# Kernel tuning notes

Measured on AMD Instinct MI355X. Metric: run time of the kernel, lower is better.

## Reference

```python
import jax, jax.numpy as jnp
import numpy as np

NPOINT, RADIUS, NSAMPLE = 1024, 0.2, 32
EPS = 1e-5


def _fps(xyz, npoint):
    # Iterative farthest point sampling (deterministic start at index 0).
    B, N, _ = xyz.shape
    def step(carry, _):
        distance, farthest = carry
        centroid = jnp.take_along_axis(xyz, farthest[:, None, None], axis=1)  # (B,1,3)
        d = jnp.sum((xyz - centroid) ** 2, -1)                                # (B,N)
        distance = jnp.minimum(distance, d)
        return (distance, jnp.argmax(distance, -1)), farthest
    init = (jnp.full((B, N), 1e10, xyz.dtype), jnp.zeros((B,), jnp.int32))
    _, idx = jax.lax.scan(step, init, None, length=npoint)
    return idx.T  # (B, npoint)


def _gather(points, idx):
    # points (B,N,C), idx (B,S,K) -> (B,S,K,C)
    B, S, K = idx.shape
    flat = jnp.take_along_axis(points, idx.reshape(B, S * K)[:, :, None], axis=1)
    return flat.reshape(B, S, K, points.shape[-1])


def _query_ball(xyz, new_xyz):
    # For each centroid, first NSAMPLE point indices within RADIUS (pad with first hit).
    B, N, _ = xyz.shape
    sqr = jnp.sum((new_xyz[:, :, None, :] - xyz[:, None, :, :]) ** 2, -1)  # (B,S,N)
    gi = jnp.where(sqr > RADIUS ** 2, N, jnp.arange(N, dtype=jnp.int32)[None, None, :])
    gi = jnp.sort(gi, axis=-1)[:, :, :NSAMPLE]
    return jnp.where(gi == N, gi[:, :, :1], gi)  # (B,S,K)


def _cond_layer(x, t_embed, wt, bt, wc, bc, g, b):
    # ConditionalConv1d: x += time_mlp(gelu(t)); 1x1 conv; BatchNorm (batch stats); GELU.
    tp = jax.nn.gelu(t_embed, approximate=False) @ wt.T + bt      # (B,Cin)
    x = x + tp[:, None, None, :]
    y = jnp.einsum('bskc,oc->bsko', x, wc) + bc                   # (B,S,K,Cout)
    mu = jnp.mean(y, axis=(0, 1, 2))
    var = jnp.var(y, axis=(0, 1, 2))
    y = (y - mu) * jax.lax.rsqrt(var + EPS) * g + b
    return jax.nn.gelu(y, approximate=False)


def _forward(xyz, points, t_embed, params):
    fps_idx = _fps(xyz, NPOINT)                                        # (B,S)
    new_xyz = jnp.take_along_axis(xyz, fps_idx[:, :, None], axis=1)    # (B,S,3)
    idx = _query_ball(xyz, new_xyz)                                    # (B,S,K)
    grouped_xyz = _gather(xyz, idx) - new_xyz[:, :, None, :]           # (B,S,K,3)
    grouped_pts = _gather(jnp.swapaxes(points, 1, 2), idx)             # (B,S,K,C)
    x = jnp.concatenate([grouped_xyz, grouped_pts], -1)                # (B,S,K,C+3)
    for p in params:
        x = _cond_layer(x, t_embed, *p)
    new_points = jnp.swapaxes(jnp.max(x, axis=2), 1, 2)                # (B,Cout,S)
    return new_xyz, new_points


def setup_inputs() -> dict:
    key = jax.random.key(0)
    ks = iter(jax.random.split(key, 32))
    B, N, CIN, T = 8, 4096, 64, 128
    chans = [(CIN + 3, 64), (64, 64), (64, 128)]
    inp = {
        "xyz": jax.random.normal(next(ks), (B, N, 3), jnp.float32),
        "points": jax.random.normal(next(ks), (B, CIN, N), jnp.float32),
        "t_embed": jax.random.normal(next(ks), (B, T), jnp.float32),
    }
    for i, (ci, co) in enumerate(chans):
        inp[f"wt{i}"] = jax.random.normal(next(ks), (ci, T), jnp.float32) * 0.05
        inp[f"bt{i}"] = jnp.zeros((ci,), jnp.float32)
        inp[f"wc{i}"] = jax.random.normal(next(ks), (co, ci), jnp.float32) * 0.1
        inp[f"bc{i}"] = jnp.zeros((co,), jnp.float32)
        inp[f"g{i}"] = jnp.ones((co,), jnp.float32)
        inp[f"be{i}"] = jnp.zeros((co,), jnp.float32)
    return inp


def reference(xyz, points, t_embed,
              wt0, bt0, wc0, bc0, g0, be0,
              wt1, bt1, wc1, bc1, g1, be1,
              wt2, bt2, wc2, bc2, g2, be2):
    params = [(wt0, bt0, wc0, bc0, g0, be0),
              (wt1, bt1, wc1, bc1, g1, be1),
              (wt2, bt2, wc2, bc2, g2, be2)]
    return _forward(xyz, points, t_embed, params)
```

## Files before the change

### kernel.cpp

```cpp
#include <hip/hip_runtime.h>
#include <cmath>

#define Bc 8
#define Nc 4096
#define Sc 1024
#define Kc 32
#define Mc (Bc*Sc*Kc)

typedef float v2f __attribute__((ext_vector_type(2)));

__device__ __forceinline__ float gelu_f(float x){
  return 0.5f*x*(1.0f + erff(x*0.70710678f));
}

__device__ __forceinline__ v2f pk_add(v2f a, v2f b){
  v2f d; asm("v_pk_add_f32 %0, %1, %2" : "=v"(d) : "v"(a), "v"(b)); return d;
}
__device__ __forceinline__ v2f pk_mul(v2f a, v2f b){
  v2f d; asm("v_pk_mul_f32 %0, %1, %2" : "=v"(d) : "v"(a), "v"(b)); return d;
}

#define ROR_MAXF(v, n) { int _t = __builtin_amdgcn_update_dpp(__float_as_int(v), __float_as_int(v), 0x120|(n), 0xF, 0xF, false); \
                         v = fmaxf(v, __int_as_float(_t)); }
#define BC15_MAXF(v)   { int _t = __builtin_amdgcn_update_dpp(__float_as_int(v), __float_as_int(v), 0x142, 0xA, 0xF, false); \
                         v = fmaxf(v, __int_as_float(_t)); }
#define BC31_MAXF(v)   { int _t = __builtin_amdgcn_update_dpp(__float_as_int(v), __float_as_int(v), 0x143, 0xC, 0xF, false); \
                         v = fmaxf(v, __int_as_float(_t)); }

#define TK(v_, i_) { const bool _t = ((v_) > Bv) || (((v_) == Bv) && ((i_) < Bi)); \
  Bv = _t ? (v_) : Bv; Bi = _t ? (i_) : Bi; }

__global__ __launch_bounds__(256) void fused_front_kernel(
    const float* __restrict__ xyz, float* __restrict__ new_xyz,
    const float* __restrict__ points, float* __restrict__ pointsT,
    const float* __restrict__ t_embed,
    const float* __restrict__ wt0, const float* __restrict__ bt0,
    const float* __restrict__ wt1, const float* __restrict__ bt1,
    const float* __restrict__ wt2, const float* __restrict__ bt2,
    float* __restrict__ tp)
{
  __shared__ __align__(16) float smem[17424];
  const int bid = blockIdx.x;
  const int tid = threadIdx.x;

  if (bid < 8){
    const int b = bid;
    const int lane = tid & 63;
    const int wv = tid >> 6;
    const float* xb = xyz + b*Nc*3;
    float*    skv   = smem;
    unsigned* ski   = (unsigned*)(smem + 8);
    int*      shist = (int*)(smem + 16);
    float4*   c4    = (float4*)(smem + 1040);

    const int base = tid << 4;
    float4 f[12];
    const float4* src = (const float4*)(xb + base*3);
#pragma unroll
    for (int q=0;q<12;++q) f[q] = src[q];
#define AR(i) ((i)%4==0 ? f[(i)/4].x : (i)%4==1 ? f[(i)/4].y : (i)%4==2 ? f[(i)/4].z : f[(i)/4].w)
    v2f px2[8], py2[8], pz2[8], d2[8];
#pragma unroll
    for (int k=0;k<8;++k){
      px2[k].x = AR(6*k+0); py2[k].x = AR(6*k+1); pz2[k].x = AR(6*k+2);
      px2[k].y = AR(6*k+3); py2[k].y = AR(6*k+4); pz2[k].y = AR(6*k+5);
      c4[base+2*k  ] = make_float4(px2[k].x, py2[k].x, pz2[k].x, 0.f);
      c4[base+2*k+1] = make_float4(px2[k].y, py2[k].y, pz2[k].y, 0.f);
      d2[k].x = 1e10f; d2[k].y = 1e10f;
    }
#undef AR
    __syncthreads();
    int widx = 0;
    for (int it=0; it<Sc; ++it){
      const float4 cc = c4[widx];
      if (tid==0) shist[it] = widx;
      v2f ncx, ncy, ncz;
      ncx.x=-cc.x; ncx.y=-cc.x; ncy.x=-cc.y; ncy.y=-cc.y; ncz.x=-cc.z; ncz.y=-cc.z;
      float bvx=-1.0f, bvy=-1.0f;
#pragma unroll
      for (int k=0;k<8;++k){
        const v2f dx = pk_add(px2[k], ncx);
        const v2f dy = pk_add(py2[k], ncy);
        const v2f dz = pk_add(pz2[k], ncz);
        const v2f dd = pk_add(pk_add(pk_mul(dx,dx), pk_mul(dy,dy)), pk_mul(dz,dz));
        v2f dn;
        dn.x = fminf(d2[k].x, dd.x);
        dn.y = fminf(d2[k].y, dd.y);
        d2[k] = dn;
        bvx = fmaxf(bvx, dn.x);
        bvy = fmaxf(bvy, dn.y);
      }
      const float bv = fmaxf(bvx, bvy);
      unsigned bi_local = 0xFFFFFFFFu;
#pragma unroll
      for (int k=0;k<8;++k){
        const unsigned c0 = (d2[k].x == bv) ? (unsigned)(base + 2*k    ) : 0xFFFFFFFFu;
        const unsigned c1 = (d2[k].y == bv) ? (unsigned)(base + 2*k + 1) : 0xFFFFFFFFu;
        const unsigned cm = (c0 < c1) ? c0 : c1;
        bi_local = (cm < bi_local) ? cm : bi_local;
      }
      float mv = bv;
      ROR_MAXF(mv,1); ROR_MAXF(mv,2); ROR_MAXF(mv,4); ROR_MAXF(mv,8);
      BC15_MAXF(mv); BC31_MAXF(mv);
      mv = __int_as_float(__builtin_amdgcn_readlane(__float_as_int(mv), 63));
      const unsigned long long mk = __ballot(bv == mv);
      const int src_lane = __ffsll(mk) - 1;
      const unsigned bi = (unsigned)__builtin_amdgcn_readlane((int)bi_local, src_lane);
      const int p4 = (it & 1) << 2;
      if (lane==0){ skv[p4+wv] = mv; ski[p4+wv] = bi; }
      __syncthreads();
      const float4 m4 = *reinterpret_cast<const float4*>(&skv[p4]);
      const uint4  i4 = *reinterpret_cast<const uint4*>(&ski[p4]);
      float Bv = m4.x; unsigned Bi = i4.x;
      TK(m4.y, i4.y) TK(m4.z, i4.z) TK(m4.w, i4.w)
      widx = (int)Bi;
    }
    __syncthreads();
    for (int i = tid; i < Sc; i += 256){
      const float4 cc = c4[shist[i]];
      float* o = new_xyz + ((size_t)b*Sc + i)*3;
      o[0]=cc.x; o[1]=cc.y; o[2]=cc.z;
    }
  } else if (bid < 520){
    const int t  = bid - 8;
    const int tb = t >> 6;
    const int n0 = (t & 63) << 6;
    float (*tile)[65] = (float(*)[65])smem;
    const int sub = tid >> 6;
    const int ln  = tid & 63;
#pragma unroll 4
    for (int cp=0; cp<16; ++cp){
      const int c = (cp<<2) + sub;
      tile[c][ln] = points[((size_t)(tb*64+c))*Nc + n0 + ln];
    }
    __syncthreads();
#pragma unroll 4
    for (int np=0; np<16; ++np){
      const int nl = (np<<2) + sub;
      pointsT[((size_t)(tb*Nc + n0 + nl))*64 + ln] = tile[ln][nl];
    }
  } else {
    float* ge = smem;
    for (int i = tid; i < Bc*128; i += 256) ge[i] = gelu_f(t_embed[i]);
    __syncthreads();
    for (int i = tid; i < 3*Bc*68; i += 256){
      const int l = i / (Bc*68);
      const int r = i - l*(Bc*68);
      const int b = r / 68;
      const int c = r - b*68;
      const int ci = (l==0) ? 67 : 64;
      float v = 0.0f;
      if (c < ci){
        const float* wt = (l==0)?wt0:((l==1)?wt1:wt2);
        const float* bt = (l==0)?bt0:((l==1)?bt1:bt2);
        const float* w = wt + c*128;
        const float* g = ge + b*128;
        float acc = 0.0f;
        for (int t2=0;t2<128;++t2) acc = fmaf(g[t2], w[t2], acc);
        v = acc + bt[c];
      }
      tp[i] = v;
    }
  }
}

__global__ __launch_bounds__(256) void ballgather_kernel(const float* __restrict__ xyz,
    const float* __restrict__ new_xyz, const float* __restrict__ pointsT,
    float* __restrict__ X){
  const int g = (blockIdx.x<<2) + (threadIdx.x>>6);
  const int lane = threadIdx.x & 63;
  const int w = threadIdx.x >> 6;
  const int b = g >> 10;
  const float* xb = xyz + b*Nc*3;
  const float cx = new_xyz[g*3+0];
  const float cy = new_xyz[g*3+1];
  const float cz = new_xyz[g*3+2];
  __shared__ int sidx[4][32];
  int total = 0;
  for (int base=0; base<Nc; base+=64){
    const int i = base + lane;
    float dx=__fsub_rn(cx, xb[i*3+0]);
    float dy=__fsub_rn(cy, xb[i*3+1]);
    float dz=__fsub_rn(cz, xb[i*3+2]);
    float sq=__fadd_rn(__fadd_rn(__fmul_rn(dx,dx),__fmul_rn(dy,dy)),__fmul_rn(dz,dz));
    bool hit = !(sq > 0.04f);
    unsigned long long m = __ballot(hit);
    if (hit){
      int pos = total + (int)__popcll(m & ((1ull<<lane)-1ull));
      if (pos < 32) sidx[w][pos] = i;
    }
    total += (int)__popcll(m);
    if (total >= 32) break;
  }
  const int fill = (total < 32) ? total : 32;
  const int first = sidx[w][0];
  if (lane >= fill && lane < 32) sidx[w][lane] = first;
  for (int k=0; k<32; ++k){
    const int pidx = sidx[w][k];
    const float* pt = pointsT + ((size_t)((b<<12)+pidx))*64;
    float* xr = X + (size_t)((g<<5)+k)*68;
    float v;
    if      (lane==0) v = __fsub_rn(xb[pidx*3+0], cx);
    else if (lane==1) v = __fsub_rn(xb[pidx*3+1], cy);
    else if (lane==2) v = __fsub_rn(xb[pidx*3+2], cz);
    else              v = pt[lane-3];
    xr[lane] = v;
    if (lane < 4){
      const int c = 64 + lane;
      xr[c] = (c<67) ? pt[c-3] : 0.0f;
    }
  }
}

template<int NORMIN, int CI_REAL, int CI_PAD, int LDX>
__global__ __launch_bounds__(256) void mm_kernel(const float* X,
    const float* __restrict__ wc, const float* __restrict__ tp,
    const float* __restrict__ sc_in, const float* __restrict__ sh_in,
    float* Y, float* __restrict__ pS, float* __restrict__ pQ, int o_base)
{
  __shared__ __align__(16) float wT[CI_PAD][64];
  __shared__ __align__(16) float tpr[CI_PAD];
  __shared__ __align__(16) float scN[64], shN[64];
  __shared__ float redS[4][64];
  __shared__ float redQ[4][64];
  const int tid = threadIdx.x;
  const int m0 = blockIdx.x << 8;
  const int b  = blockIdx.x >> 7;
  for (int idx = tid; idx < CI_PAD*64; idx += 256){
    int c = idx >> 6, o = idx & 63;
    wT[c][o] = (c < CI_REAL) ? wc[(o_base + o)*CI_REAL + c] : 0.0f;
  }
  if (tid < CI_PAD) tpr[tid] = tp[b*68 + tid];
  if (NORMIN && tid < 64){ scN[tid] = sc_in[tid]; shN[tid] = sh_in[tid]; }
  __syncthreads();
  const int rg = tid >> 2, cg = tid & 3;
  const float* x0 = X + (size_t)(m0 + (rg<<2)) * LDX;
  float4 acc[4][4];
#pragma unroll
  for (int r=0;r<4;++r)
#pragma unroll
    for (int q=0;q<4;++q) acc[r][q] = make_float4(0.f,0.f,0.f,0.f);

  float4 xpf[4];
#pragma unroll
  for (int r=0;r<4;++r) xpf[r] = *reinterpret_cast<const float4*>(x0 + r*LDX);

#pragma unroll 1
  for (int c = 0; c < CI_PAD; c += 4){
    float4 xc[4];
#pragma unroll
    for (int r=0;r<4;++r) xc[r] = xpf[r];
    if (c + 4 < CI_PAD){
#pragma unroll
      for (int r=0;r<4;++r) xpf[r] = *reinterpret_cast<const float4*>(x0 + r*LDX + (c+4));
    }
    const float4 tpv = *reinterpret_cast<const float4*>(&tpr[c]);
    if (NORMIN){
      const float4 sci = *reinterpret_cast<const float4*>(&scN[c]);
      const float4 shi = *reinterpret_cast<const float4*>(&shN[c]);
#pragma unroll
      for (int r=0;r<4;++r){
        xc[r].x = gelu_f(fmaf(xc[r].x, sci.x, shi.x));
        xc[r].y = gelu_f(fmaf(xc[r].y, sci.y, shi.y));
        xc[r].z = gelu_f(fmaf(xc[r].z, sci.z, shi.z));
        xc[r].w = gelu_f(fmaf(xc[r].w, sci.w, shi.w));
      }
    }
    float4 xr[4];
#pragma unroll
    for (int r=0;r<4;++r)
      xr[r] = make_float4(xc[r].x+tpv.x, xc[r].y+tpv.y, xc[r].z+tpv.z, xc[r].w+tpv.w);
#pragma unroll
    for (int cc=0; cc<4; ++cc){
      const float* wrow = &wT[c+cc][cg<<4];
      const float4 w0 = *reinterpret_cast<const float4*>(wrow);
      const float4 w1 = *reinterpret_cast<const float4*>(wrow+4);
      const float4 w2 = *reinterpret_cast<const float4*>(wrow+8);
      const float4 w3 = *reinterpret_cast<const float4*>(wrow+12);
#pragma unroll
      for (int r=0;r<4;++r){
        const float xs = (cc==0)?xr[r].x:((cc==1)?xr[r].y:((cc==2)?xr[r].z:xr[r].w));
        acc[r][0].x = fmaf(xs, w0.x, acc[r][0].x);
        acc[r][0].y = fmaf(xs, w0.y, acc[r][0].y);
        acc[r][0].z = fmaf(xs, w0.z, acc[r][0].z);
        acc[r][0].w = fmaf(xs, w0.w, acc[r][0].w);
        acc[r][1].x = fmaf(xs, w1.x, acc[r][1].x);
        acc[r][1].y = fmaf(xs, w1.y, acc[r][1].y);
        acc[r][1].z = fmaf(xs, w1.z, acc[r][1].z);
        acc[r][1].w = fmaf(xs, w1.w, acc[r][1].w);
        acc[r][2].x = fmaf(xs, w2.x, acc[r][2].x);
        acc[r][2].y = fmaf(xs, w2.y, acc[r][2].y);
        acc[r][2].z = fmaf(xs, w2.z, acc[r][2].z);
        acc[r][2].w = fmaf(xs, w2.w, acc[r][2].w);
        acc[r][3].x = fmaf(xs, w3.x, acc[r][3].x);
        acc[r][3].y = fmaf(xs, w3.y, acc[r][3].y);
        acc[r][3].z = fmaf(xs, w3.z, acc[r][3].z);
        acc[r][3].w = fmaf(xs, w3.w, acc[r][3].w);
      }
    }
  }
#pragma unroll
  for (int r=0;r<4;++r){
    float4* yp = reinterpret_cast<float4*>(Y + (size_t)(m0 + (rg<<2) + r)*64 + (cg<<4));
#pragma unroll
    for (int q=0;q<4;++q) yp[q] = acc[r][q];
  }
  float4 s[4], q2[4];
#pragma unroll
  for (int q=0;q<4;++q){
    float sx=0,sy=0,sz=0,sw=0, qx=0,qy=0,qz=0,qw=0;
#pragma unroll
    for (int r=0;r<4;++r){
      sx+=acc[r][q].x; qx+=acc[r][q].x*acc[r][q].x;
      sy+=acc[r][q].y; qy+=acc[r][q].y*acc[r][q].y;
      sz+=acc[r][q].z; qz+=acc[r][q].z*acc[r][q].z;
      sw+=acc[r][q].w; qw+=acc[r][q].w*acc[r][q].w;
    }
    s[q]=make_float4(sx,sy,sz,sw); q2[q]=make_float4(qx,qy,qz,qw);
  }
  const int lane = tid & 63, wvv = tid >> 6;
#pragma unroll
  for (int off=32; off>=4; off>>=1){
#pragma unroll
    for (int q=0;q<4;++q){
      s[q].x  += __shfl_down(s[q].x,  off);
      s[q].y  += __shfl_down(s[q].y,  off);
      s[q].z  += __shfl_down(s[q].z,  off);
      s[q].w  += __shfl_down(s[q].w,  off);
      q2[q].x += __shfl_down(q2[q].x, off);
      q2[q].y += __shfl_down(q2[q].y, off);
      q2[q].z += __shfl_down(q2[q].z, off);
      q2[q].w += __shfl_down(q2[q].w, off);
    }
  }
  if (lane < 4){
#pragma unroll
    for (int q=0;q<4;++q){
      redS[wvv][lane*16 + q*4 + 0] = s[q].x;
      redS[wvv][lane*16 + q*4 + 1] = s[q].y;
      redS[wvv][lane*16 + q*4 + 2] = s[q].z;
      redS[wvv][lane*16 + q*4 + 3] = s[q].w;
      redQ[wvv][lane*16 + q*4 + 0] = q2[q].x;
      redQ[wvv][lane*16 + q*4 + 1] = q2[q].y;
      redQ[wvv][lane*16 + q*4 + 2] = q2[q].z;
      redQ[wvv][lane*16 + q*4 + 3] = q2[q].w;
    }
  }
  __syncthreads();
  if (tid < 64){
    float a=0.f, bb=0.f;
#pragma unroll
    for (int w2=0; w2<4; ++w2){ a += redS[w2][tid]; bb += redQ[w2][tid]; }
    pS[(blockIdx.x<<6) + tid] = a;
    pQ[(blockIdx.x<<6) + tid] = bb;
  }
}

__global__ __launch_bounds__(256) void mm2_kernel(const float* X,
    const float* __restrict__ wc, const float* __restrict__ tp,
    const float* __restrict__ sc_in, const float* __restrict__ sh_in,
    float* Y0, float* Y1, float* __restrict__ pS, float* __restrict__ pQ)
{
  __shared__ __align__(16) float wT[64][128];
  __shared__ __align__(16) float tpr[64];
  __shared__ __align__(16) float scN[64], shN[64];
  __shared__ float redS[4][128];
  __shared__ float redQ[4][128];
  const int tid = threadIdx.x;
  const int m0 = blockIdx.x << 7;
  const int b  = blockIdx.x >> 8;
  for (int idx = tid; idx < 64*128; idx += 256){
    const int c = idx >> 7, o = idx & 127;
    wT[c][o] = wc[o*64 + c];
  }
  if (tid < 64) tpr[tid] = tp[b*68 + tid];
  else if (tid < 128) scN[tid-64] = sc_in[tid-64];
  else if (tid < 192) shN[tid-128] = sh_in[tid-128];
  __syncthreads();
  const int rg = tid >> 2, cg = tid & 3;
  const int cb = cg << 2;
  const float* x0 = X + (size_t)(m0 + (rg<<1)) * 64;
  float4 acc[2][8];
#pragma unroll
  for (int r=0;r<2;++r)
#pragma unroll
    for (int q=0;q<8;++q) acc[r][q] = make_float4(0.f,0.f,0.f,0.f);

  float4 xpf[2];
  xpf[0] = *reinterpret_cast<const float4*>(x0);
  xpf[1] = *reinterpret_cast<const float4*>(x0 + 64);

#pragma unroll 1
  for (int c = 0; c < 64; c += 4){
    float4 xc[2]; xc[0]=xpf[0]; xc[1]=xpf[1];
    if (c + 4 < 64){
      xpf[0] = *reinterpret_cast<const float4*>(x0 + (c+4));
      xpf[1] = *reinterpret_cast<const float4*>(x0 + 64 + (c+4));
    }
    const float4 tpv = *reinterpret_cast<const float4*>(&tpr[c]);
    const float4 sci = *reinterpret_cast<const float4*>(&scN[c]);
    const float4 shi = *reinterpret_cast<const float4*>(&shN[c]);
#pragma unroll
    for (int r=0;r<2;++r){
      xc[r].x = gelu_f(fmaf(xc[r].x, sci.x, shi.x)) + tpv.x;
      xc[r].y = gelu_f(fmaf(xc[r].y, sci.y, shi.y)) + tpv.y;
      xc[r].z = gelu_f(fmaf(xc[r].z, sci.z, shi.z)) + tpv.z;
      xc[r].w = gelu_f(fmaf(xc[r].w, sci.w, shi.w)) + tpv.w;
    }
#pragma unroll
    for (int cc=0; cc<4; ++cc){
      const float xs0 = (cc==0)?xc[0].x:((cc==1)?xc[0].y:((cc==2)?xc[0].z:xc[0].w));
      const float xs1 = (cc==0)?xc[1].x:((cc==1)?xc[1].y:((cc==2)?xc[1].z:xc[1].w));
      const float* wrow = &wT[c+cc][cb];
#pragma unroll
      for (int j=0;j<8;++j){
        const float4 wv = *reinterpret_cast<const float4*>(wrow + (j<<4));
        acc[0][j].x = fmaf(xs0, wv.x, acc[0][j].x);
        acc[0][j].y = fmaf(xs0, wv.y, acc[0][j].y);
        acc[0][j].z = fmaf(xs0, wv.z, acc[0][j].z);
        acc[0][j].w = fmaf(xs0, wv.w, acc[0][j].w);
        acc[1][j].x = fmaf(xs1, wv.x, acc[1][j].x);
        acc[1][j].y = fmaf(xs1, wv.y, acc[1][j].y);
        acc[1][j].z = fmaf(xs1, wv.z, acc[1][j].z);
        acc[1][j].w = fmaf(xs1, wv.w, acc[1][j].w);
      }
    }
  }
#pragma unroll
  for (int r=0;r<2;++r){
    const size_t row = (size_t)(m0 + (rg<<1) + r);
#pragma unroll
    for (int j=0;j<8;++j){
      float* yb = (j<4) ? Y0 : Y1;
      const int col = ((j<4) ? (j<<4) : ((j-4)<<4)) + cb;
      *reinterpret_cast<float4*>(yb + row*64 + col) = acc[r][j];
    }
  }
  const int lane = tid & 63, wvv = tid >> 6;
#pragma unroll
  for (int j=0;j<8;++j){
    float4 s = make_float4(acc[0][j].x+acc[1][j].x, acc[0][j].y+acc[1][j].y,
                           acc[0][j].z+acc[1][j].z, acc[0][j].w+acc[1][j].w);
    float4 q2 = make_float4(acc[0][j].x*acc[0][j].x + acc[1][j].x*acc[1][j].x,
                            acc[0][j].y*acc[0][j].y + acc[1][j].y*acc[1][j].y,
                            acc[0][j].z*acc[0][j].z + acc[1][j].z*acc[1][j].z,
                            acc[0][j].w*acc[0][j].w + acc[1][j].w*acc[1][j].w);
#pragma unroll
    for (int off=32; off>=4; off>>=1){
      s.x += __shfl_down(s.x, off);   s.y += __shfl_down(s.y, off);
      s.z += __shfl_down(s.z, off);   s.w += __shfl_down(s.w, off);
      q2.x += __shfl_down(q2.x, off); q2.y += __shfl_down(q2.y, off);
      q2.z += __shfl_down(q2.z, off); q2.w += __shfl_down(q2.w, off);
    }
    if (lane < 4){
      const int ch = (j<<4) + (lane<<2);
      redS[wvv][ch+0]=s.x;  redS[wvv][ch+1]=s.y;  redS[wvv][ch+2]=s.z;  redS[wvv][ch+3]=s.w;
      redQ[wvv][ch+0]=q2.x; redQ[wvv][ch+1]=q2.y; redQ[wvv][ch+2]=q2.z; redQ[wvv][ch+3]=q2.w;
    }
  }
  __syncthreads();
  if (tid < 128){
    float a=0.f, bb=0.f;
#pragma unroll
    for (int w2=0; w2<4; ++w2){ a += redS[w2][tid]; bb += redQ[w2][tid]; }
    pS[(size_t)blockIdx.x*128 + tid] = a;
    pQ[(size_t)blockIdx.x*128 + tid] = bb;
  }
}

template<int CO>
__global__ __launch_bounds__(1024) void finalize_kernel(const float* __restrict__ pS,
    const float* __restrict__ pQ, const float* __restrict__ g, const float* __restrict__ be,
    float* __restrict__ scale, float* __restrict__ shift, int nblk){
  __shared__ float rS[1024], rQ[1024];
  constexpr int NCH = 1024 / CO;
  const int o  = threadIdx.x & (CO-1);
  const int ch = threadIdx.x / CO;
  const int per = nblk / NCH;
  const int i0 = ch * per;
  float s=0.f, q=0.f;
#pragma unroll 4
  for (int i=0;i<per;++i){
    s += pS[(size_t)(i0+i)*CO + o];
    q += pQ[(size_t)(i0+i)*CO + o];
  }
  rS[threadIdx.x]=s; rQ[threadIdx.x]=q;
  __syncthreads();
  if (threadIdx.x < CO){
    float ss = 0.f, qq = 0.f;
#pragma unroll
    for (int c=0;c<NCH;++c){ ss += rS[c*CO+o]; qq += rQ[c*CO+o]; }
    const float inv_n = 1.0f/(float)Mc;
    const float mu = ss*inv_n;
    const float var = qq*inv_n - mu*mu;
    const float rs = 1.0f/sqrtf(var + 1e-5f);
    const float sc = rs*g[o];
    scale[o] = sc;
    shift[o] = fmaf(-mu, sc, be[o]);
  }
}

__global__ __launch_bounds__(256) void pool_kernel(const float* __restrict__ Y,
    const float* __restrict__ scale, const float* __restrict__ shift,
    float* __restrict__ out, int o_base){
  __shared__ float pool[32][65];
  const int tid = threadIdx.x;
  const int b  = blockIdx.x >> 5;
  const int s0 = (blockIdx.x & 31) << 5;
  const int c  = tid & 63;
  const int sl0 = tid >> 6;
  const float sc = scale[c], sh = shift[c];
  for (int sp=0; sp<8; ++sp){
    const int sl = (sp<<2) + sl0;
    const int s = s0 + sl;
    const float* yp = Y + ((size_t)((b<<10)+s)<<5)*64 + c;
    float mx = -1e30f;
#pragma unroll 4
    for (int k=0;k<32;++k){
      float v = yp[(size_t)(k<<6)];
      v = gelu_f(fmaf(v, sc, sh));
      mx = fmaxf(mx, v);
    }
    pool[sl][c] = mx;
  }
  __syncthreads();
  for (int p=0;p<8;++p){
    const int c2 = (p<<3) + (tid>>5);
    const int sl = tid & 31;
    out[((size_t)((b<<7) + o_base + c2)<<10) + s0 + sl] = pool[sl][c2];
  }
}

extern "C" void kernel_launch(void* const* d_in, const int* in_sizes, int n_in,
                              void* d_out, int out_size, void* d_ws, size_t ws_size,
                              hipStream_t stream){
  const float* xyz     = (const float*)d_in[0];
  const float* points  = (const float*)d_in[1];
  const float* t_embed = (const float*)d_in[2];
  const float* wt0=(const float*)d_in[3],  *bt0=(const float*)d_in[4],  *wc0=(const float*)d_in[5];
  const float* g0 =(const float*)d_in[7],  *be0=(const float*)d_in[8];
  const float* wt1=(const float*)d_in[9],  *bt1=(const float*)d_in[10], *wc1=(const float*)d_in[11];
  const float* g1 =(const float*)d_in[13], *be1=(const float*)d_in[14];
  const float* wt2=(const float*)d_in[15], *bt2=(const float*)d_in[16], *wc2=(const float*)d_in[17];
  const float* g2 =(const float*)d_in[19], *be2=(const float*)d_in[20];

  float* out_xyz = (float*)d_out;
  float* out_pts = (float*)d_out + Bc*Sc*3;

  float* ws       = (float*)d_ws;
  float* tp       = ws + 0;
  float* pointsT  = ws + 2048;
  float* pS       = ws + 2099200;
  float* X        = ws + 2361344;
  float* Ya       = ws + 20187136;
  float* pQ       = ws + 36964352;
  float* sc0      = ws + 37226496;
  float* sh0      = sc0 + 64;
  float* sc1      = sc0 + 128;
  float* sh1      = sc0 + 192;
  float* sc2      = sc0 + 256;
  float* sh2      = sc0 + 384;
  float* Yx       = X;

  const int NBLK = Mc/256;

  fused_front_kernel<<<521, 256, 0, stream>>>(xyz, out_xyz, points, pointsT,
      t_embed, wt0,bt0, wt1,bt1, wt2,bt2, tp);
  ballgather_kernel<<<(Bc*Sc)/4, 256, 0, stream>>>(xyz, out_xyz, pointsT, X);

  mm_kernel<0,67,68,68><<<NBLK, 256, 0, stream>>>(X, wc0, tp, nullptr, nullptr, Ya, pS, pQ, 0);
  finalize_kernel<64><<<1, 1024, 0, stream>>>(pS, pQ, g0, be0, sc0, sh0, NBLK);

  mm_kernel<1,64,64,64><<<NBLK, 256, 0, stream>>>(Ya, wc1, tp + 544, sc0, sh0, Ya, pS, pQ, 0);
  finalize_kernel<64><<<1, 1024, 0, stream>>>(pS, pQ, g1, be1, sc1, sh1, NBLK);

  mm2_kernel<<<Mc/128, 256, 0, stream>>>(Ya, wc2, tp + 1088, sc1, sh1, Yx, Ya, pS, pQ);
  finalize_kernel<128><<<1, 1024, 0, stream>>>(pS, pQ, g2, be2, sc2, sh2, Mc/128);

  pool_kernel<<<Bc*Sc/32, 256, 0, stream>>>(Yx, sc2,    sh2,    out_pts, 0);
  pool_kernel<<<Bc*Sc/32, 256, 0, stream>>>(Ya, sc2+64, sh2+64, out_pts, 64);
}
```

Baseline: 1.176 ms.

## Halve mm_kernel row tile, deepen X prefetch, merge pool launches

mm_kernel now has each block cover 128 rows, with 2 rows per thread instead of 4. That doubles the block count and cuts accumulator registers, aiming for more occupancy and better latency hiding. Both mm_kernel and mm2_kernel now prefetch two 4-channel chunks of X ahead instead of one, to overlap global loads with FMA work. The two pool_kernel launches become a single launch that picks its input half from the block index. In exchange, each weight value loaded from LDS now feeds fewer FMAs, and there are twice as many partial BN statistics for finalize to reduce.

```diff
diff --git a/kernel.cpp b/kernel.cpp
--- a/kernel.cpp
+++ b/kernel.cpp
@@ -212,6 +212,54 @@
   }
 }
 
+#define MM_CHUNK(CB, XV)                                                            \
+  {                                                                                 \
+    const float4 tpv = *reinterpret_cast<const float4*>(&tpr[CB]);                  \
+    if (NORMIN){                                                                    \
+      const float4 sci = *reinterpret_cast<const float4*>(&scN[CB]);                \
+      const float4 shi = *reinterpret_cast<const float4*>(&shN[CB]);                \
+      _Pragma("unroll")                                                             \
+      for (int r=0;r<2;++r){                                                        \
+        XV[r].x = gelu_f(fmaf(XV[r].x, sci.x, shi.x));                              \
+        XV[r].y = gelu_f(fmaf(XV[r].y, sci.y, shi.y));                              \
+        XV[r].z = gelu_f(fmaf(XV[r].z, sci.z, shi.z));                              \
+        XV[r].w = gelu_f(fmaf(XV[r].w, sci.w, shi.w));                              \
+      }                                                                             \
+    }                                                                               \
+    _Pragma("unroll")                                                               \
+    for (int r=0;r<2;++r){                                                          \
+      XV[r].x += tpv.x; XV[r].y += tpv.y; XV[r].z += tpv.z; XV[r].w += tpv.w;       \
+    }                                                                               \
+    _Pragma("unroll")                                                               \
+    for (int cc=0; cc<4; ++cc){                                                     \
+      const float* wrow = &wT[(CB)+cc][cg<<4];                                      \
+      const float4 w0 = *reinterpret_cast<const float4*>(wrow);                     \
+      const float4 w1 = *reinterpret_cast<const float4*>(wrow+4);                   \
+      const float4 w2 = *reinterpret_cast<const float4*>(wrow+8);                   \
+      const float4 w3 = *reinterpret_cast<const float4*>(wrow+12);                  \
+      _Pragma("unroll")                                                             \
+      for (int r=0;r<2;++r){                                                        \
+        const float xs = (cc==0)?XV[r].x:((cc==1)?XV[r].y:((cc==2)?XV[r].z:XV[r].w));\
+        acc[r][0].x = fmaf(xs, w0.x, acc[r][0].x);                                  \
+        acc[r][0].y = fmaf(xs, w0.y, acc[r][0].y);                                  \
+        acc[r][0].z = fmaf(xs, w0.z, acc[r][0].z);                                  \
+        acc[r][0].w = fmaf(xs, w0.w, acc[r][0].w);                                  \
+        acc[r][1].x = fmaf(xs, w1.x, acc[r][1].x);                                  \
+        acc[r][1].y = fmaf(xs, w1.y, acc[r][1].y);                                  \
+        acc[r][1].z = fmaf(xs, w1.z, acc[r][1].z);                                  \
+        acc[r][1].w = fmaf(xs, w1.w, acc[r][1].w);                                  \
+        acc[r][2].x = fmaf(xs, w2.x, acc[r][2].x);                                  \
+        acc[r][2].y = fmaf(xs, w2.y, acc[r][2].y);                                  \
+        acc[r][2].z = fmaf(xs, w2.z, acc[r][2].z);                                  \
+        acc[r][2].w = fmaf(xs, w2.w, acc[r][2].w);                                  \
+        acc[r][3].x = fmaf(xs, w3.x, acc[r][3].x);                                  \
+        acc[r][3].y = fmaf(xs, w3.y, acc[r][3].y);                                  \
+        acc[r][3].z = fmaf(xs, w3.z, acc[r][3].z);                                  \
+        acc[r][3].w = fmaf(xs, w3.w, acc[r][3].w);                                  \
+      }                                                                             \
+    }                                                                               \
+  }
+
 template<int NORMIN, int CI_REAL, int CI_PAD, int LDX>
 __global__ __launch_bounds__(256) void mm_kernel(const float* X,
     const float* __restrict__ wc, const float* __restrict__ tp,
@@ -224,8 +272,8 @@
   __shared__ float redS[4][64];
   __shared__ float redQ[4][64];
   const int tid = threadIdx.x;
-  const int m0 = blockIdx.x << 8;
-  const int b  = blockIdx.x >> 7;
+  const int m0 = blockIdx.x << 7;
+  const int b  = blockIdx.x >> 8;
   for (int idx = tid; idx < CI_PAD*64; idx += 256){
     int c = idx >> 6, o = idx & 63;
     wT[c][o] = (c < CI_REAL) ? wc[(o_base + o)*CI_REAL + c] : 0.0f;
@@ -234,89 +282,51 @@
   if (NORMIN && tid < 64){ scN[tid] = sc_in[tid]; shN[tid] = sh_in[tid]; }
   __syncthreads();
   const int rg = tid >> 2, cg = tid & 3;
-  const float* x0 = X + (size_t)(m0 + (rg<<2)) * LDX;
-  float4 acc[4][4];
-#pragma unroll
-  for (int r=0;r<4;++r)
+  const float* x0 = X + (size_t)(m0 + (rg<<1)) * LDX;
+  float4 acc[2][4];
+#pragma unroll
+  for (int r=0;r<2;++r)
 #pragma unroll
     for (int q=0;q<4;++q) acc[r][q] = make_float4(0.f,0.f,0.f,0.f);
 
-  float4 xpf[4];
-#pragma unroll
-  for (int r=0;r<4;++r) xpf[r] = *reinterpret_cast<const float4*>(x0 + r*LDX);
+  float4 pfA[2], pfB[2];
+  pfA[0] = *reinterpret_cast<const float4*>(x0);
+  pfA[1] = *reinterpret_cast<const float4*>(x0 + LDX);
+  pfB[0] = *reinterpret_cast<const float4*>(x0 + 4);
+  pfB[1] = *reinterpret_cast<const float4*>(x0 + LDX + 4);
 
 #pragma unroll 1
-  for (int c = 0; c < CI_PAD; c += 4){
-    float4 xc[4];
-#pragma unroll
-    for (int r=0;r<4;++r) xc[r] = xpf[r];
+  for (int c = 0; c < CI_PAD; c += 8){
+    float4 xa[2]; xa[0]=pfA[0]; xa[1]=pfA[1];
+    if (c + 8 < CI_PAD){
+      pfA[0] = *reinterpret_cast<const float4*>(x0 + (c+8));
+      pfA[1] = *reinterpret_cast<const float4*>(x0 + LDX + (c+8));
+    }
+    MM_CHUNK(c, xa)
     if (c + 4 < CI_PAD){
-#pragma unroll
-      for (int r=0;r<4;++r) xpf[r] = *reinterpret_cast<const float4*>(x0 + r*LDX + (c+4));
-    }
-    const float4 tpv = *reinterpret_cast<const float4*>(&tpr[c]);
-    if (NORMIN){
-      const float4 sci = *reinterpret_cast<const float4*>(&scN[c]);
-      const float4 shi = *reinterpret_cast<const float4*>(&shN[c]);
-#pragma unroll
-      for (int r=0;r<4;++r){
-        xc[r].x = gelu_f(fmaf(xc[r].x, sci.x, shi.x));
-        xc[r].y = gelu_f(fmaf(xc[r].y, sci.y, shi.y));
-        xc[r].z = gelu_f(fmaf(xc[r].z, sci.z, shi.z));
-        xc[r].w = gelu_f(fmaf(xc[r].w, sci.w, shi.w));
+      float4 xb2[2]; xb2[0]=pfB[0]; xb2[1]=pfB[1];
+      if (c + 12 < CI_PAD){
+        pfB[0] = *reinterpret_cast<const float4*>(x0 + (c+12));
+        pfB[1] = *reinterpret_cast<const float4*>(x0 + LDX + (c+12));
       }
-    }
-    float4 xr[4];
-#pragma unroll
-    for (int r=0;r<4;++r)
-      xr[r] = make_float4(xc[r].x+tpv.x, xc[r].y+tpv.y, xc[r].z+tpv.z, xc[r].w+tpv.w);
-#pragma unroll
-    for (int cc=0; cc<4; ++cc){
-      const float* wrow = &wT[c+cc][cg<<4];
-      const float4 w0 = *reinterpret_cast<const float4*>(wrow);
-      const float4 w1 = *reinterpret_cast<const float4*>(wrow+4);
-      const float4 w2 = *reinterpret_cast<const float4*>(wrow+8);
-      const float4 w3 = *reinterpret_cast<const float4*>(wrow+12);
-#pragma unroll
-      for (int r=0;r<4;++r){
-        const float xs = (cc==0)?xr[r].x:((cc==1)?xr[r].y:((cc==2)?xr[r].z:xr[r].w));
-        acc[r][0].x = fmaf(xs, w0.x, acc[r][0].x);
-        acc[r][0].y = fmaf(xs, w0.y, acc[r][0].y);
-        acc[r][0].z = fmaf(xs, w0.z, acc[r][0].z);
-        acc[r][0].w = fmaf(xs, w0.w, acc[r][0].w);
-        acc[r][1].x = fmaf(xs, w1.x, acc[r][1].x);
-        acc[r][1].y = fmaf(xs, w1.y, acc[r][1].y);
-        acc[r][1].z = fmaf(xs, w1.z, acc[r][1].z);
-        acc[r][1].w = fmaf(xs, w1.w, acc[r][1].w);
-        acc[r][2].x = fmaf(xs, w2.x, acc[r][2].x);
-        acc[r][2].y = fmaf(xs, w2.y, acc[r][2].y);
-        acc[r][2].z = fmaf(xs, w2.z, acc[r][2].z);
-        acc[r][2].w = fmaf(xs, w2.w, acc[r][2].w);
-        acc[r][3].x = fmaf(xs, w3.x, acc[r][3].x);
-        acc[r][3].y = fmaf(xs, w3.y, acc[r][3].y);
-        acc[r][3].z = fmaf(xs, w3.z, acc[r][3].z);
-        acc[r][3].w = fmaf(xs, w3.w, acc[r][3].w);
-      }
-    }
-  }
-#pragma unroll
-  for (int r=0;r<4;++r){
-    float4* yp = reinterpret_cast<float4*>(Y + (size_t)(m0 + (rg<<2) + r)*64 + (cg<<4));
+      MM_CHUNK(c+4, xb2)
+    }
+  }
+#pragma unroll
+  for (int r=0;r<2;++r){
+    float4* yp = reinterpret_cast<float4*>(Y + (size_t)(m0 + (rg<<1) + r)*64 + (cg<<4));
 #pragma unroll
     for (int q=0;q<4;++q) yp[q] = acc[r][q];
   }
   float4 s[4], q2[4];
 #pragma unroll
   for (int q=0;q<4;++q){
-    float sx=0,sy=0,sz=0,sw=0, qx=0,qy=0,qz=0,qw=0;
-#pragma unroll
-    for (int r=0;r<4;++r){
-      sx+=acc[r][q].x; qx+=acc[r][q].x*acc[r][q].x;
-      sy+=acc[r][q].y; qy+=acc[r][q].y*acc[r][q].y;
-      sz+=acc[r][q].z; qz+=acc[r][q].z*acc[r][q].z;
-      sw+=acc[r][q].w; qw+=acc[r][q].w*acc[r][q].w;
-    }
-    s[q]=make_float4(sx,sy,sz,sw); q2[q]=make_float4(qx,qy,qz,qw);
+    s[q]  = make_float4(acc[0][q].x+acc[1][q].x, acc[0][q].y+acc[1][q].y,
+                        acc[0][q].z+acc[1][q].z, acc[0][q].w+acc[1][q].w);
+    q2[q] = make_float4(acc[0][q].x*acc[0][q].x + acc[1][q].x*acc[1][q].x,
+                        acc[0][q].y*acc[0][q].y + acc[1][q].y*acc[1][q].y,
+                        acc[0][q].z*acc[0][q].z + acc[1][q].z*acc[1][q].z,
+                        acc[0][q].w*acc[0][q].w + acc[1][q].w*acc[1][q].w);
   }
   const int lane = tid & 63, wvv = tid >> 6;
 #pragma unroll
@@ -351,8 +361,8 @@
     float a=0.f, bb=0.f;
 #pragma unroll
     for (int w2=0; w2<4; ++w2){ a += redS[w2][tid]; bb += redQ[w2][tid]; }
-    pS[(blockIdx.x<<6) + tid] = a;
-    pQ[(blockIdx.x<<6) + tid] = bb;
+    pS[((size_t)blockIdx.x<<6) + tid] = a;
+    pQ[((size_t)blockIdx.x<<6) + tid] = bb;
   }
 }
 
@@ -386,45 +396,58 @@
 #pragma unroll
     for (int q=0;q<8;++q) acc[r][q] = make_float4(0.f,0.f,0.f,0.f);
 
-  float4 xpf[2];
-  xpf[0] = *reinterpret_cast<const float4*>(x0);
-  xpf[1] = *reinterpret_cast<const float4*>(x0 + 64);
+#define MM2_CHUNK(CB, XV)                                                          \
+  {                                                                                \
+    const float4 tpv = *reinterpret_cast<const float4*>(&tpr[CB]);                 \
+    const float4 sci = *reinterpret_cast<const float4*>(&scN[CB]);                 \
+    const float4 shi = *reinterpret_cast<const float4*>(&shN[CB]);                 \
+    _Pragma("unroll")                                                              \
+    for (int r=0;r<2;++r){                                                         \
+      XV[r].x = gelu_f(fmaf(XV[r].x, sci.x, shi.x)) + tpv.x;                       \
+      XV[r].y = gelu_f(fmaf(XV[r].y, sci.y, shi.y)) + tpv.y;                       \
+      XV[r].z = gelu_f(fmaf(XV[r].z, sci.z, shi.z)) + tpv.z;                       \
+      XV[r].w = gelu_f(fmaf(XV[r].w, sci.w, shi.w)) + tpv.w;                       \
+    }                                                                              \
+    _Pragma("unroll")                                                              \
+    for (int cc=0; cc<4; ++cc){                                                    \
+      const float xs0 = (cc==0)?XV[0].x:((cc==1)?XV[0].y:((cc==2)?XV[0].z:XV[0].w));\
+      const float xs1 = (cc==0)?XV[1].x:((cc==1)?XV[1].y:((cc==2)?XV[1].z:XV[1].w));\
+      const float* wrow = &wT[(CB)+cc][cb];                                        \
+      _Pragma("unroll")                                                            \
+      for (int j=0;j<8;++j){                                                       \
+        const float4 wv = *reinterpret_cast<const float4*>(wrow + (j<<4));         \
+        acc[0][j].x = fmaf(xs0, wv.x, acc[0][j].x);                                \
+        acc[0][j].y = fmaf(xs0, wv.y, acc[0][j].y);                                \
+        acc[0][j].z = fmaf(xs0, wv.z, acc[0][j].z);                                \
+        acc[0][j].w = fmaf(xs0, wv.w, acc[0][j].w);                                \
+        acc[1][j].x = fmaf(xs1, wv.x, acc[1][j].x);                                \
+        acc[1][j].y = fmaf(xs1, wv.y, acc[1][j].y);                                \
+        acc[1][j].z = fmaf(xs1, wv.z, acc[1][j].z);                                \
+        acc[1][j].w = fmaf(xs1, wv.w, acc[1][j].w);                                \
+      }                                                                            \
+    }                                                                              \
+  }
+
+  float4 pfA[2], pfB[2];
+  pfA[0] = *reinterpret_cast<const float4*>(x0);
+  pfA[1] = *reinterpret_cast<const float4*>(x0 + 64);
+  pfB[0] = *reinterpret_cast<const float4*>(x0 + 4);
+  pfB[1] = *reinterpret_cast<const float4*>(x0 + 64 + 4);
 
 #pragma unroll 1
-  for (int c = 0; c < 64; c += 4){
-    float4 xc[2]; xc[0]=xpf[0]; xc[1]=xpf[1];
-    if (c + 4 < 64){
-      xpf[0] = *reinterpret_cast<const float4*>(x0 + (c+4));
-      xpf[1] = *reinterpret_cast<const float4*>(x0 + 64 + (c+4));
-    }
-    const float4 tpv = *reinterpret_cast<const float4*>(&tpr[c]);
-    const float4 sci = *reinterpret_cast<const float4*>(&scN[c]);
-    const float4 shi = *reinterpret_cast<const float4*>(&shN[c]);
-#pragma unroll
-    for (int r=0;r<2;++r){
-      xc[r].x = gelu_f(fmaf(xc[r].x, sci.x, shi.x)) + tpv.x;
-      xc[r].y = gelu_f(fmaf(xc[r].y, sci.y, shi.y)) + tpv.y;
-      xc[r].z = gelu_f(fmaf(xc[r].z, sci.z, shi.z)) + tpv.z;
-      xc[r].w = gelu_f(fmaf(xc[r].w, sci.w, shi.w)) + tpv.w;
-    }
-#pragma unroll
-    for (int cc=0; cc<4; ++cc){
-      const float xs0 = (cc==0)?xc[0].x:((cc==1)?xc[0].y:((cc==2)?xc[0].z:xc[0].w));
-      const float xs1 = (cc==0)?xc[1].x:((cc==1)?xc[1].y:((cc==2)?xc[1].z:xc[1].w));
-      const float* wrow = &wT[c+cc][cb];
-#pragma unroll
-      for (int j=0;j<8;++j){
-        const float4 wv = *reinterpret_cast<const float4*>(wrow + (j<<4));
-        acc[0][j].x = fmaf(xs0, wv.x, acc[0][j].x);
-        acc[0][j].y = fmaf(xs0, wv.y, acc[0][j].y);
-        acc[0][j].z = fmaf(xs0, wv.z, acc[0][j].z);
-        acc[0][j].w = fmaf(xs0, wv.w, acc[0][j].w);
-        acc[1][j].x = fmaf(xs1, wv.x, acc[1][j].x);
-        acc[1][j].y = fmaf(xs1, wv.y, acc[1][j].y);
-        acc[1][j].z = fmaf(xs1, wv.z, acc[1][j].z);
-        acc[1][j].w = fmaf(xs1, wv.w, acc[1][j].w);
-      }
-    }
+  for (int c = 0; c < 64; c += 8){
+    float4 xa[2]; xa[0]=pfA[0]; xa[1]=pfA[1];
+    if (c + 8 < 64){
+      pfA[0] = *reinterpret_cast<const float4*>(x0 + (c+8));
+      pfA[1] = *reinterpret_cast<const float4*>(x0 + 64 + (c+8));
+    }
+    MM2_CHUNK(c, xa)
+    float4 xb2[2]; xb2[0]=pfB[0]; xb2[1]=pfB[1];
+    if (c + 12 < 64){
+      pfB[0] = *reinterpret_cast<const float4*>(x0 + (c+12));
+      pfB[1] = *reinterpret_cast<const float4*>(x0 + 64 + (c+12));
+    }
+    MM2_CHUNK(c+4, xb2)
   }
 #pragma unroll
   for (int r=0;r<2;++r){
@@ -500,16 +523,19 @@
   }
 }
 
-__global__ __launch_bounds__(256) void pool_kernel(const float* __restrict__ Y,
-    const float* __restrict__ scale, const float* __restrict__ shift,
-    float* __restrict__ out, int o_base){
+__global__ __launch_bounds__(256) void pool_kernel(const float* __restrict__ Y0,
+    const float* __restrict__ Y1, const float* __restrict__ scale,
+    const float* __restrict__ shift, float* __restrict__ out){
   __shared__ float pool[32][65];
   const int tid = threadIdx.x;
-  const int b  = blockIdx.x >> 5;
-  const int s0 = (blockIdx.x & 31) << 5;
+  const int half = blockIdx.x >> 8;
+  const float* Y = half ? Y1 : Y0;
+  const int bb = blockIdx.x & 255;
+  const int b  = bb >> 5;
+  const int s0 = (bb & 31) << 5;
   const int c  = tid & 63;
   const int sl0 = tid >> 6;
-  const float sc = scale[c], sh = shift[c];
+  const float sc = scale[(half<<6) + c], sh = shift[(half<<6) + c];
   for (int sp=0; sp<8; ++sp){
     const int sl = (sp<<2) + sl0;
     const int s = s0 + sl;
@@ -527,7 +553,7 @@
   for (int p=0;p<8;++p){
     const int c2 = (p<<3) + (tid>>5);
     const int sl = tid & 31;
-    out[((size_t)((b<<7) + o_base + c2)<<10) + s0 + sl] = pool[sl][c2];
+    out[((size_t)((b<<7) + (half<<6) + c2)<<10) + s0 + sl] = pool[sl][c2];
   }
 }
 
@@ -562,7 +588,7 @@
   float* sh2      = sc0 + 384;
   float* Yx       = X;
 
-  const int NBLK = Mc/256;
+  const int NBLK = Mc/128;
 
   fused_front_kernel<<<521, 256, 0, stream>>>(xyz, out_xyz, points, pointsT,
       t_embed, wt0,bt0, wt1,bt1, wt2,bt2, tp);
@@ -577,6 +603,5 @@
   mm2_kernel<<<Mc/128, 256, 0, stream>>>(Ya, wc2, tp + 1088, sc1, sh1, Yx, Ya, pS, pQ);
   finalize_kernel<128><<<1, 1024, 0, stream>>>(pS, pQ, g2, be2, sc2, sh2, Mc/128);
 
-  pool_kernel<<<Bc*Sc/32, 256, 0, stream>>>(Yx, sc2,    sh2,    out_pts, 0);
-  pool_kernel<<<Bc*Sc/32, 256, 0, stream>>>(Ya, sc2+64, sh2+64, out_pts, 64);
-}
+  pool_kernel<<<512, 256, 0, stream>>>(Yx, Ya, sc2, sh2, out_pts);
+}
```

After: 1.217 ms. +3.5%, slower.
